# Optimization experiments

Hardware: AMD Instinct MI355X
Metric: run time of the kernel (lower is better)

## Reference

```python
import jax, jax.numpy as jnp
import numpy as np

N = 50000        # nodes
E = 800000       # edges
H = 256          # hidden_dim == output_dim
L = 5            # num_layers
NUM_ATOM_F = 9   # OGB atom categorical features
NUM_BOND_F = 3   # OGB bond categorical features
ATOM_VOCAB = 64
BOND_VOCAB = 8
G = 128          # num graphs in batch
BN_EPS = 1e-5


def setup_inputs() -> dict:
    key = jax.random.key(0)
    ks = jax.random.split(key, 24)
    s = 0.02
    inp = {
        "x_feat": jax.random.randint(ks[0], (N, NUM_ATOM_F), 0, ATOM_VOCAB),
        "edge_index": jax.random.randint(ks[1], (2, E), 0, N),
        "edge_attr_raw": jax.random.randint(ks[2], (E, NUM_BOND_F), 0, BOND_VOCAB),
        "batch": jnp.sort(jax.random.randint(ks[3], (N,), 0, G)),
        "atom_emb": s * jax.random.normal(ks[4], (NUM_ATOM_F, ATOM_VOCAB, H), jnp.float32),
        "bond_emb": s * jax.random.normal(ks[5], (NUM_BOND_F, BOND_VOCAB, H), jnp.float32),
        # per-layer GINEConv MLP: Linear(H,H) -> BN -> relu -> Linear(H,H) -> relu
        "W1": s * jax.random.normal(ks[6], (L, H, H), jnp.float32),
        "b1": jnp.zeros((L, H), jnp.float32),
        "g1": jnp.ones((L, H), jnp.float32),
        "be1": jnp.zeros((L, H), jnp.float32),
        "W2": s * jax.random.normal(ks[7], (L, H, H), jnp.float32),
        "b2": jnp.zeros((L, H), jnp.float32),
        # outer per-layer BN
        "g2": jnp.ones((L, H), jnp.float32),
        "be2": jnp.zeros((L, H), jnp.float32),
        # output head: Linear -> BN -> relu -> Linear
        "outW1": s * jax.random.normal(ks[8], (H, H), jnp.float32),
        "outb1": jnp.zeros((H,), jnp.float32),
        "outg": jnp.ones((H,), jnp.float32),
        "outbe": jnp.zeros((H,), jnp.float32),
        "outW2": s * jax.random.normal(ks[9], (H, H), jnp.float32),
        "outb2": jnp.zeros((H,), jnp.float32),
    }
    return inp


def _bn(x, g, b):
    mu = jnp.mean(x, axis=0)
    var = jnp.var(x, axis=0)
    return (x - mu) * jax.lax.rsqrt(var + BN_EPS) * g + b


def reference(x_feat, edge_index, edge_attr_raw, batch,
              atom_emb, bond_emb, W1, b1, g1, be1, W2, b2, g2, be2,
              outW1, outb1, outg, outbe, outW2, outb2):
    # Atom/Bond encoders: sum of per-feature embeddings
    x = sum(atom_emb[f][x_feat[:, f]] for f in range(NUM_ATOM_F))        # [N,H]
    e = sum(bond_emb[f][edge_attr_raw[:, f]] for f in range(NUM_BOND_F))  # [E,H]
    src, dst = edge_index[0], edge_index[1]

    for i in range(L):
        # GINEConv: (1+eps)*x + sum_j relu(x_j + e_ij), eps=0
        m = jax.nn.relu(x[src] + e)                       # [E,H]
        agg = jax.ops.segment_sum(m, dst, num_segments=N)  # [N,H]
        h = x + agg
        h = jax.nn.relu(_bn(h @ W1[i] + b1[i], g1[i], be1[i]))
        h = jax.nn.relu(h @ W2[i] + b2[i])
        x = jax.nn.relu(_bn(h, g2[i], be2[i]))

    # output head + global_add_pool
    h = jax.nn.relu(_bn(x @ outW1 + outb1, outg, outbe))
    h = h @ outW2 + outb2
    return jax.ops.segment_sum(h, batch, num_segments=G)   # [G,H]
```

## Files before the change

kernel.cpp:

```cpp
#include <hip/hip_runtime.h>
#include <hip/hip_bf16.h>

#define NN 50000
#define EE 800000
#define HH 256
#define GG 128
#define LL 5
#define NCHUNK 196
#define BN_EPS 1e-5f

typedef __attribute__((ext_vector_type(8))) short short8_t;
typedef __attribute__((ext_vector_type(4))) float f32x4;
typedef __hip_bfloat16 bf16;

#define AS1 __attribute__((address_space(1)))
#define AS3 __attribute__((address_space(3)))

__device__ __forceinline__ float bf2f(unsigned short u) {
    unsigned int i = ((unsigned int)u) << 16;
    float f;
    __builtin_memcpy(&f, &i, 4);
    return f;
}
__device__ __forceinline__ unsigned short f2bf(float f) {
    bf16 h = __float2bfloat16(f);
    unsigned short u;
    __builtin_memcpy(&u, &h, 2);
    return u;
}

__global__ __launch_bounds__(256) void k_encode(const int* __restrict__ xf,
                                                const float* __restrict__ atom_emb,
                                                bf16* __restrict__ x) {
    int n = blockIdx.x, h = threadIdx.x;
    float s = 0.f;
#pragma unroll
    for (int f = 0; f < 9; ++f) {
        int v = xf[n * 9 + f];
        s += atom_emb[((size_t)f * 64 + v) * HH + h];
    }
    x[(size_t)n * HH + h] = __float2bfloat16(s);
}

__global__ __launch_bounds__(256) void k_combo(const float* __restrict__ bond_emb,
                                               bf16* __restrict__ table) {
    int c = blockIdx.x, h = threadIdx.x;
    float v = bond_emb[(size_t)((c >> 6) & 7) * HH + h]
            + bond_emb[(size_t)(8 + ((c >> 3) & 7)) * HH + h]
            + bond_emb[(size_t)(16 + (c & 7)) * HH + h];
    table[(size_t)c * HH + h] = __float2bfloat16(v);
}

__global__ __launch_bounds__(256) void k_prepw(const float* __restrict__ W1,
                                               const float* __restrict__ W2,
                                               const float* __restrict__ oW1,
                                               const float* __restrict__ oW2,
                                               bf16* __restrict__ out) {
    int z = blockIdx.z;
    const float* src = (z < 5) ? W1 + (size_t)z * 65536
                     : (z < 10) ? W2 + (size_t)(z - 5) * 65536
                     : (z == 10) ? oW1 : oW2;
    bf16* dst = out + (size_t)z * 65536;
    __shared__ float tile[32][33];
    int kt = blockIdx.y * 32, nt = blockIdx.x * 32;
    int tx = threadIdx.x, ty = threadIdx.y;
    for (int i = ty; i < 32; i += 8) tile[i][tx] = src[(size_t)(kt + i) * 256 + nt + tx];
    __syncthreads();
    for (int i = ty; i < 32; i += 8)
        dst[(size_t)(nt + i) * 256 + kt + tx] = __float2bfloat16(tile[tx][i]);
}

__global__ __launch_bounds__(256) void k_hist(const int* __restrict__ ei, int* __restrict__ deg) {
    int e = blockIdx.x * 256 + threadIdx.x;
    if (e < EE) atomicAdd(&deg[ei[EE + e]], 1);
}

__global__ __launch_bounds__(256) void k_scan_a(const int* __restrict__ deg, int* __restrict__ ro,
                                                int* __restrict__ bsum) {
    __shared__ int sm[256];
    int b = blockIdx.x, t = threadIdx.x;
    int idx = b * 256 + t;
    int v = (idx < NN) ? deg[idx] : 0;
    sm[t] = v;
    __syncthreads();
    for (int off = 1; off < 256; off <<= 1) {
        int add = (t >= off) ? sm[t - off] : 0;
        __syncthreads();
        sm[t] += add;
        __syncthreads();
    }
    if (idx <= NN) ro[idx] = sm[t] - v;
    if (t == 255) bsum[b] = sm[255];
}

__global__ __launch_bounds__(256) void k_scan_b(int* __restrict__ bsum) {
    __shared__ int sm[256];
    int t = threadIdx.x;
    int v = (t < NCHUNK) ? bsum[t] : 0;
    sm[t] = v;
    __syncthreads();
    for (int off = 1; off < 256; off <<= 1) {
        int add = (t >= off) ? sm[t - off] : 0;
        __syncthreads();
        sm[t] += add;
        __syncthreads();
    }
    if (t < NCHUNK) bsum[t] = sm[t] - v;
}

__global__ __launch_bounds__(256) void k_scan_c(int* __restrict__ ro, const int* __restrict__ bsum,
                                                int* __restrict__ cursor) {
    int b = blockIdx.x, t = threadIdx.x;
    int idx = b * 256 + t;
    if (idx <= NN) {
        int val = ro[idx] + bsum[b];
        ro[idx] = val;
        if (idx < NN) cursor[idx] = val;
    }
}

__global__ __launch_bounds__(256) void k_scatter(const int* __restrict__ ei,
                                                 const int* __restrict__ attr,
                                                 int* __restrict__ cursor,
                                                 int2* __restrict__ ebuf) {
    int e = blockIdx.x * 256 + threadIdx.x;
    if (e < EE) {
        int d = ei[EE + e];
        int c = (attr[e * 3] << 6) | (attr[e * 3 + 1] << 3) | attr[e * 3 + 2];
        int pos = atomicAdd(&cursor[d], 1);
        ebuf[pos] = make_int2(ei[e], c);
    }
}

__global__ __launch_bounds__(256) void k_bnrelu(bf16* __restrict__ t,
                                                const float* __restrict__ sIn,
                                                const float* __restrict__ qIn,
                                                const float* __restrict__ gIn,
                                                const float* __restrict__ beIn,
                                                float invN) {
    int grp = threadIdx.x >> 6;
    int lane = threadIdx.x & 63;
    int h4 = lane * 4;
    float4 s4 = *(const float4*)(sIn + h4);
    float4 q4 = *(const float4*)(qIn + h4);
    float4 g4 = *(const float4*)(gIn + h4);
    float4 b4 = *(const float4*)(beIn + h4);
    float4 cav, cbv;
#define COEF(C)                                                 \
    { float mu = s4.C * invN;                                   \
      float var = fmaf(-mu, mu, q4.C * invN);                   \
      float a = g4.C * rsqrtf(var + BN_EPS);                    \
      cav.C = a; cbv.C = fmaf(-mu, a, b4.C); }
    COEF(x) COEF(y) COEF(z) COEF(w)
#undef COEF
    int n = blockIdx.x * 4 + grp;
    if (n >= NN) return;
    ushort4 v = *(const ushort4*)(t + (size_t)n * HH + h4);
    ushort4 o;
    o.x = f2bf(fmaxf(fmaf(bf2f(v.x), cav.x, cbv.x), 0.f));
    o.y = f2bf(fmaxf(fmaf(bf2f(v.y), cav.y, cbv.y), 0.f));
    o.z = f2bf(fmaxf(fmaf(bf2f(v.z), cav.z, cbv.z), 0.f));
    o.w = f2bf(fmaxf(fmaf(bf2f(v.w), cav.w, cbv.w), 0.f));
    *(ushort4*)(t + (size_t)n * HH + h4) = o;
}

__global__ __launch_bounds__(256) void k_aggregate(const bf16* __restrict__ u,
                                                   const int* __restrict__ ro,
                                                   const int2* __restrict__ eb,
                                                   const bf16* __restrict__ combo,
                                                   bf16* __restrict__ aggout) {
    int wid = threadIdx.x >> 6;
    int lane = threadIdx.x & 63;
    int half = lane >> 5;
    int sl = lane & 31;
    int n = blockIdx.x * 4 + wid;
    if (n >= NN) return;
    int h8 = sl * 8;
    float p0[8] = {0.f, 0.f, 0.f, 0.f, 0.f, 0.f, 0.f, 0.f};
    float p1[8] = {0.f, 0.f, 0.f, 0.f, 0.f, 0.f, 0.f, 0.f};
    int e0 = ro[n], e1 = ro[n + 1];
    int j = e0;
#define ACCUM(P, xs, cs)                                                       \
    {                                                                          \
        unsigned int xw[4] = {xs.x, xs.y, xs.z, xs.w};                         \
        unsigned int cw[4] = {cs.x, cs.y, cs.z, cs.w};                         \
        _Pragma("unroll") for (int q = 0; q < 4; ++q) {                        \
            float xlo = __uint_as_float(xw[q] << 16);                          \
            float xhi = __uint_as_float(xw[q] & 0xffff0000u);                  \
            float clo = __uint_as_float(cw[q] << 16);                          \
            float chi = __uint_as_float(cw[q] & 0xffff0000u);                  \
            P[2 * q] += fmaxf(xlo + clo, 0.f);                                 \
            P[2 * q + 1] += fmaxf(xhi + chi, 0.f);                             \
        }                                                                      \
    }
    for (; j + 4 <= e1; j += 4) {
        int2 rA = eb[j + half];
        int2 rB = eb[j + 2 + half];
        uint4 xA = *(const uint4*)(u + (size_t)rA.x * HH + h8);
        uint4 cA = *(const uint4*)(combo + ((size_t)rA.y << 8) + h8);
        uint4 xB = *(const uint4*)(u + (size_t)rB.x * HH + h8);
        uint4 cB = *(const uint4*)(combo + ((size_t)rB.y << 8) + h8);
        ACCUM(p0, xA, cA);
        ACCUM(p1, xB, cB);
    }
    for (; j < e1; j += 2) {
        int idx = j + half;
        bool v = idx < e1;
        int2 r = eb[v ? idx : e0];
        uint4 xA = *(const uint4*)(u + (size_t)r.x * HH + h8);
        uint4 cA = *(const uint4*)(combo + ((size_t)r.y << 8) + h8);
        if (v) ACCUM(p0, xA, cA);
    }
#undef ACCUM
#pragma unroll
    for (int i = 0; i < 8; ++i) {
        p0[i] += p1[i];
        p0[i] += __shfl_xor(p0[i], 32);
    }
    if (half == 0) {
        uint4 tv = *(const uint4*)(u + (size_t)n * HH + h8);
        unsigned int tw[4] = {tv.x, tv.y, tv.z, tv.w};
        unsigned int ow[4];
#pragma unroll
        for (int q = 0; q < 4; ++q) {
            float tlo = __uint_as_float(tw[q] << 16);
            float thi = __uint_as_float(tw[q] & 0xffff0000u);
            ow[q] = (unsigned int)f2bf(p0[2 * q] + tlo)
                  | ((unsigned int)f2bf(p0[2 * q + 1] + thi) << 16);
        }
        *(uint4*)(aggout + (size_t)n * HH + h8) = make_uint4(ow[0], ow[1], ow[2], ow[3]);
    }
}

struct GLds {
    uint4 a[2][512];
    uint4 b[2][1024];
    float ca[256], cb[256];
};

__device__ __forceinline__ uint4 xchunk(uint4 u, const float* ca, const float* cb, int k0) {
    float4 ca0 = *(const float4*)(ca + k0);
    float4 ca1 = *(const float4*)(ca + k0 + 4);
    float4 cb0 = *(const float4*)(cb + k0);
    float4 cb1 = *(const float4*)(cb + k0 + 4);
    float cav[8] = {ca0.x, ca0.y, ca0.z, ca0.w, ca1.x, ca1.y, ca1.z, ca1.w};
    float cbv[8] = {cb0.x, cb0.y, cb0.z, cb0.w, cb1.x, cb1.y, cb1.z, cb1.w};
    unsigned int s[4] = {u.x, u.y, u.z, u.w};
#pragma unroll
    for (int p = 0; p < 4; ++p) {
        float lo = bf2f((unsigned short)(s[p] & 0xffffu));
        float hi = bf2f((unsigned short)(s[p] >> 16));
        lo = fmaxf(fmaf(lo, cav[2 * p], cbv[2 * p]), 0.f);
        hi = fmaxf(fmaf(hi, cav[2 * p + 1], cbv[2 * p + 1]), 0.f);
        s[p] = (unsigned int)f2bf(lo) | ((unsigned int)f2bf(hi) << 16);
    }
    return make_uint4(s[0], s[1], s[2], s[3]);
}

template <bool HAS_T, bool POOL>
__global__ __launch_bounds__(512, 4) void k_gemm(const bf16* __restrict__ A,
                                                 const bf16* __restrict__ Wt,
                                                 const float* __restrict__ bias,
                                                 bf16* __restrict__ Out,
                                                 int M, int do_relu,
                                                 const float* __restrict__ sIn,
                                                 const float* __restrict__ qIn,
                                                 const float* __restrict__ gIn,
                                                 const float* __restrict__ beIn,
                                                 float invN,
                                                 float* __restrict__ ssum,
                                                 float* __restrict__ ssq,
                                                 const int* __restrict__ pbatch,
                                                 float* __restrict__ pout) {
    __shared__ GLds L;
    const int t = threadIdx.x;
    const int lane = t & 63;
    const int w = t >> 6;
    const int wr = w >> 2, wc = w & 3;
    const int m0 = blockIdx.x * 128;
    const int lhi = lane >> 4, llo = lane & 15;

    if (HAS_T) {
        if (t < 256) {
            float mu = sIn[t] * invN;
            float var = fmaf(-mu, mu, qIn[t] * invN);
            float a = gIn[t] * rsqrtf(var + BN_EPS);
            L.ca[t] = a;
            L.cb[t] = fmaf(-mu, a, beIn[t]);
        }
        __syncthreads();
    }

    const int arow_i = t & 127, akg = t >> 7;
    const bf16* aptr = A + (size_t)(m0 + arow_i) * HH + akg * 8;
    const int bcol = wc * 64 + lane;
    const bf16* bptr = Wt + (size_t)bcol * HH + wr * 8;

    f32x4 acc[4][4] = {};
    uint4 areg, anext;

#define STAGE_B(c, kb)                                                                        \
    _Pragma("unroll") for (int q = 0; q < 2; ++q) {                                           \
        __builtin_amdgcn_global_load_lds((const AS1 void*)(bptr + (kb) + q * 16),             \
                                         (AS3 void*)&L.b[c][q * 512 + w * 64], 16, 0, 0);     \
    }
#define STAGE_A_DMA(c, kb)                                                                    \
    __builtin_amdgcn_global_load_lds((const AS1 void*)(aptr + (kb)),                          \
                                     (AS3 void*)&L.a[c][w * 64], 16, 0, 0);

    STAGE_B(0, 0);
    if (HAS_T) {
        areg = *(const uint4*)(aptr + 0);
        L.a[0][t] = xchunk(areg, L.ca, L.cb, akg * 8);
    } else {
        STAGE_A_DMA(0, 0);
    }
    __syncthreads();

    int c = 0;
    for (int step = 0; step < 8; ++step) {
        const int kn = (step + 1) * 32;
        if (step < 7) {
            STAGE_B(c ^ 1, kn);
            if (HAS_T) anext = *(const uint4*)(aptr + kn);
            else STAGE_A_DMA(c ^ 1, kn);
        }
        short8_t af[4], bfv[4];
#pragma unroll
        for (int m = 0; m < 4; ++m)
            af[m] = *(const short8_t*)&L.a[c][lhi * 128 + wr * 64 + m * 16 + llo];
#pragma unroll
        for (int n = 0; n < 4; ++n)
            bfv[n] = *(const short8_t*)&L.b[c][lhi * 256 + wc * 64 + n * 16 + llo];
#pragma unroll
        for (int m = 0; m < 4; ++m)
#pragma unroll
            for (int n = 0; n < 4; ++n)
                acc[m][n] = __builtin_amdgcn_mfma_f32_16x16x32_bf16(af[m], bfv[n], acc[m][n], 0, 0, 0);
        if (HAS_T && step < 7)
            L.a[c ^ 1][t] = xchunk(anext, L.ca, L.cb, kn + akg * 8);
        __syncthreads();
        c ^= 1;
    }
#undef STAGE_B
#undef STAGE_A_DMA

    float bias_n[4];
    int col_n[4];
#pragma unroll
    for (int n = 0; n < 4; ++n) {
        col_n[n] = wc * 64 + n * 16 + llo;
        bias_n[n] = bias[col_n[n]];
    }

    if (POOL) {
        int gcur = -1;
        float pacc[4] = {0.f, 0.f, 0.f, 0.f};
#pragma unroll
        for (int m = 0; m < 4; ++m) {
#pragma unroll
            for (int j = 0; j < 4; ++j) {
                int row = m0 + wr * 64 + m * 16 + lhi * 4 + j;
                if (row < M) {
                    int g = pbatch[row];
                    if (g != gcur) {
                        if (gcur >= 0) {
#pragma unroll
                            for (int n = 0; n < 4; ++n)
                                atomicAdd(&pout[(size_t)gcur * HH + col_n[n]], pacc[n]);
                        }
                        gcur = g;
#pragma unroll
                        for (int n = 0; n < 4; ++n) pacc[n] = 0.f;
                    }
#pragma unroll
                    for (int n = 0; n < 4; ++n)
                        pacc[n] += acc[m][n][j] + bias_n[n];
                }
            }
        }
        if (gcur >= 0) {
#pragma unroll
            for (int n = 0; n < 4; ++n)
                atomicAdd(&pout[(size_t)gcur * HH + col_n[n]], pacc[n]);
        }
        return;
    }

    float ps[4] = {0.f, 0.f, 0.f, 0.f}, pq[4] = {0.f, 0.f, 0.f, 0.f};
#pragma unroll
    for (int m = 0; m < 4; ++m) {
#pragma unroll
        for (int j = 0; j < 4; ++j) {
            int row = m0 + wr * 64 + m * 16 + lhi * 4 + j;
            bool valid = row < M;
#pragma unroll
            for (int n = 0; n < 4; ++n) {
                float v = acc[m][n][j] + bias_n[n];
                if (do_relu) v = fmaxf(v, 0.f);
                if (valid) {
                    Out[(size_t)row * HH + col_n[n]] = __float2bfloat16(v);
                    ps[n] += v;
                    pq[n] = fmaf(v, v, pq[n]);
                }
            }
        }
    }

    if (ssum) {
#pragma unroll
        for (int n = 0; n < 4; ++n) {
            float s = ps[n];
            s += __shfl_xor(s, 16);
            s += __shfl_xor(s, 32);
            float q = pq[n];
            q += __shfl_xor(q, 16);
            q += __shfl_xor(q, 32);
            if (lhi == 0) {
                atomicAdd(&ssum[col_n[n]], s);
                atomicAdd(&ssq[col_n[n]], q);
            }
        }
    }
}

static size_t align256(size_t v) { return (v + 255) & ~(size_t)255; }

extern "C" void kernel_launch(void* const* d_in, const int* in_sizes, int n_in,
                              void* d_out, int out_size, void* d_ws, size_t ws_size,
                              hipStream_t stream) {
    const int* x_feat = (const int*)d_in[0];
    const int* ei = (const int*)d_in[1];
    const int* attr = (const int*)d_in[2];
    const int* batch = (const int*)d_in[3];
    const float* atom_emb = (const float*)d_in[4];
    const float* bond_emb = (const float*)d_in[5];
    const float* W1 = (const float*)d_in[6];
    const float* b1 = (const float*)d_in[7];
    const float* g1 = (const float*)d_in[8];
    const float* be1 = (const float*)d_in[9];
    const float* W2 = (const float*)d_in[10];
    const float* b2 = (const float*)d_in[11];
    const float* g2 = (const float*)d_in[12];
    const float* be2 = (const float*)d_in[13];
    const float* outW1 = (const float*)d_in[14];
    const float* outb1 = (const float*)d_in[15];
    const float* outg = (const float*)d_in[16];
    const float* outbe = (const float*)d_in[17];
    const float* outW2 = (const float*)d_in[18];
    const float* outb2 = (const float*)d_in[19];
    float* out = (float*)d_out;

    char* ws = (char*)d_ws;
    const size_t BUF_STRIDE = align256((size_t)NN * HH * 2 + 131072);
    bf16* bufA = (bf16*)ws;
    bf16* bufB = (bf16*)(ws + BUF_STRIDE);
    bf16* bufC = (bf16*)(ws + 2 * BUF_STRIDE);
    char* p = ws + 3 * BUF_STRIDE;
    int2* ebuf = (int2*)p;            p += align256((size_t)EE * sizeof(int2));
    int* deg = (int*)p;
    float* stats = (float*)(p + (size_t)NN * sizeof(int));
    const size_t ZERO_BYTES = (size_t)NN * sizeof(int) + 11 * 512 * sizeof(float);
    p += align256(ZERO_BYTES);
    int* ro = (int*)p;                p += align256((size_t)(NN + 1) * sizeof(int));
    int* cursor = (int*)p;            p += align256((size_t)NN * sizeof(int));
    int* bsum = (int*)p;              p += align256(256 * sizeof(int));
    bf16* combo = (bf16*)p;           p += align256((size_t)512 * HH * sizeof(bf16));
    bf16* wbuf = (bf16*)p;            p += align256((size_t)12 * 65536 * sizeof(bf16));

    const float invN = 1.0f / (float)NN;
    const int EBLK = (EE + 255) / 256;
    const int GBLK = (NN + 127) / 128;
    const int AGG_GRID = (NN + 3) / 4;
    const int BNR_GRID = (NN + 3) / 4;

    hipMemsetAsync(deg, 0, ZERO_BYTES, stream);
    k_hist<<<EBLK, 256, 0, stream>>>(ei, deg);
    k_scan_a<<<NCHUNK, 256, 0, stream>>>(deg, ro, bsum);
    k_scan_b<<<1, 256, 0, stream>>>(bsum);
    k_scan_c<<<NCHUNK, 256, 0, stream>>>(ro, bsum, cursor);
    k_scatter<<<EBLK, 256, 0, stream>>>(ei, attr, cursor, ebuf);
    k_combo<<<512, 256, 0, stream>>>(bond_emb, combo);
    k_prepw<<<dim3(8, 8, 12), dim3(32, 8), 0, stream>>>(W1, W2, outW1, outW2, wbuf);
    k_encode<<<NN, 256, 0, stream>>>(x_feat, atom_emb, bufA);

    for (int l = 0; l < LL; ++l) {
        float* s1 = stats + (size_t)(2 * l) * 512;
        float* q1 = s1 + 256;
        float* s2 = stats + (size_t)(2 * l + 1) * 512;
        float* q2 = s2 + 256;
        if (l > 0) {
            float* sp = stats + (size_t)(2 * l - 1) * 512;
            k_bnrelu<<<BNR_GRID, 256, 0, stream>>>(bufA, sp, sp + 256,
                                                   g2 + (size_t)(l - 1) * HH,
                                                   be2 + (size_t)(l - 1) * HH, invN);
        }
        k_aggregate<<<AGG_GRID, 256, 0, stream>>>(bufA, ro, ebuf, combo, bufB);
        k_gemm<false, false><<<GBLK, 512, 0, stream>>>(bufB, wbuf + (size_t)l * 65536,
                                                       b1 + (size_t)l * HH, bufC, NN, 0,
                                                       nullptr, nullptr, nullptr, nullptr,
                                                       invN, s1, q1, nullptr, nullptr);
        k_gemm<true, false><<<GBLK, 512, 0, stream>>>(bufC, wbuf + (size_t)(5 + l) * 65536,
                                                      b2 + (size_t)l * HH, bufA, NN, 1,
                                                      s1, q1, g1 + (size_t)l * HH,
                                                      be1 + (size_t)l * HH, invN, s2, q2,
                                                      nullptr, nullptr);
    }

    float* sP = stats + (size_t)9 * 512;
    float* sH = stats + (size_t)10 * 512;
    float* qH = sH + 256;
    k_bnrelu<<<BNR_GRID, 256, 0, stream>>>(bufA, sP, sP + 256,
                                           g2 + (size_t)4 * HH, be2 + (size_t)4 * HH, invN);
    k_gemm<false, false><<<GBLK, 512, 0, stream>>>(bufA, wbuf + (size_t)10 * 65536, outb1,
                                                   bufB, NN, 0, nullptr, nullptr, nullptr,
                                                   nullptr, invN, sH, qH, nullptr, nullptr);
    hipMemsetAsync(d_out, 0, (size_t)GG * HH * sizeof(float), stream);
    k_gemm<true, true><<<GBLK, 512, 0, stream>>>(bufB, wbuf + (size_t)11 * 65536, outb2,
                                                 bufC, NN, 0, sH, qH, outg, outbe,
                                                 invN, nullptr, nullptr, batch, out);
}
```

Baseline: 941.2 us.

## Load GEMM A fragments directly to registers and fuse final BN-ReLU into head GEMM

Adds a GEMM variant for the untransformed input that loads A fragments straight from global memory into registers, skipping the LDS staging of A. This saves LDS traffic and bank pressure, but the per-lane global loads are less coalesced. The last standalone BN+ReLU pass is folded into the first head GEMM via its on-the-fly transform, which removes one full read and write of the node features. The output memset also moves to the start of the stream.

```diff
diff --git a/kernel.cpp b/kernel.cpp
--- a/kernel.cpp
+++ b/kernel.cpp
@@ -232,6 +232,111 @@
     }
 }
 
+__global__ __launch_bounds__(512, 4) void k_gemmF(const bf16* __restrict__ A,
+                                                  const bf16* __restrict__ Wt,
+                                                  const float* __restrict__ bias,
+                                                  bf16* __restrict__ Out,
+                                                  int M,
+                                                  float* __restrict__ ssum,
+                                                  float* __restrict__ ssq) {
+    __shared__ uint4 Lb[2][1024];
+    const int t = threadIdx.x;
+    const int lane = t & 63;
+    const int w = t >> 6;
+    const int wr = w >> 2, wc = w & 3;
+    const int m0 = blockIdx.x * 128;
+    const int lhi = lane >> 4, llo = lane & 15;
+
+    const int bcol = wc * 64 + lane;
+    const bf16* bptr = Wt + (size_t)bcol * HH + wr * 8;
+
+    size_t abase[4];
+#pragma unroll
+    for (int m = 0; m < 4; ++m)
+        abase[m] = (size_t)(m0 + wr * 64 + m * 16 + llo) * HH + lhi * 8;
+
+    f32x4 acc[4][4] = {};
+    uint4 ar[4], nar[4];
+
+#define STAGE_B(c, kb)                                                                        \
+    _Pragma("unroll") for (int q = 0; q < 2; ++q) {                                           \
+        __builtin_amdgcn_global_load_lds((const AS1 void*)(bptr + (kb) + q * 16),             \
+                                         (AS3 void*)&Lb[c][q * 512 + w * 64], 16, 0, 0);      \
+    }
+
+    STAGE_B(0, 0);
+#pragma unroll
+    for (int m = 0; m < 4; ++m) ar[m] = *(const uint4*)(A + abase[m]);
+    __syncthreads();
+
+    int c = 0;
+    for (int step = 0; step < 8; ++step) {
+        const int kn = (step + 1) * 32;
+        if (step < 7) {
+            STAGE_B(c ^ 1, kn);
+#pragma unroll
+            for (int m = 0; m < 4; ++m) nar[m] = *(const uint4*)(A + abase[m] + kn);
+        }
+        short8_t af[4], bfv[4];
+#pragma unroll
+        for (int m = 0; m < 4; ++m) __builtin_memcpy(&af[m], &ar[m], 16);
+#pragma unroll
+        for (int n = 0; n < 4; ++n)
+            bfv[n] = *(const short8_t*)&Lb[c][lhi * 256 + wc * 64 + n * 16 + llo];
+#pragma unroll
+        for (int m = 0; m < 4; ++m)
+#pragma unroll
+            for (int n = 0; n < 4; ++n)
+                acc[m][n] = __builtin_amdgcn_mfma_f32_16x16x32_bf16(af[m], bfv[n], acc[m][n], 0, 0, 0);
+        if (step < 7) {
+#pragma unroll
+            for (int m = 0; m < 4; ++m) ar[m] = nar[m];
+        }
+        __syncthreads();
+        c ^= 1;
+    }
+#undef STAGE_B
+
+    float bias_n[4];
+    int col_n[4];
+#pragma unroll
+    for (int n = 0; n < 4; ++n) {
+        col_n[n] = wc * 64 + n * 16 + llo;
+        bias_n[n] = bias[col_n[n]];
+    }
+    float ps[4] = {0.f, 0.f, 0.f, 0.f}, pq[4] = {0.f, 0.f, 0.f, 0.f};
+#pragma unroll
+    for (int m = 0; m < 4; ++m) {
+#pragma unroll
+        for (int j = 0; j < 4; ++j) {
+            int row = m0 + wr * 64 + m * 16 + lhi * 4 + j;
+            bool valid = row < M;
+#pragma unroll
+            for (int n = 0; n < 4; ++n) {
+                float v = acc[m][n][j] + bias_n[n];
+                if (valid) {
+                    Out[(size_t)row * HH + col_n[n]] = __float2bfloat16(v);
+                    ps[n] += v;
+                    pq[n] = fmaf(v, v, pq[n]);
+                }
+            }
+        }
+    }
+#pragma unroll
+    for (int n = 0; n < 4; ++n) {
+        float s = ps[n];
+        s += __shfl_xor(s, 16);
+        s += __shfl_xor(s, 32);
+        float q = pq[n];
+        q += __shfl_xor(q, 16);
+        q += __shfl_xor(q, 32);
+        if (lhi == 0) {
+            atomicAdd(&ssum[col_n[n]], s);
+            atomicAdd(&ssq[col_n[n]], q);
+        }
+    }
+}
+
 struct GLds {
     uint4 a[2][512];
     uint4 b[2][1024];
@@ -257,21 +362,21 @@
     return make_uint4(s[0], s[1], s[2], s[3]);
 }
 
-template <bool HAS_T, bool POOL>
-__global__ __launch_bounds__(512, 4) void k_gemm(const bf16* __restrict__ A,
-                                                 const bf16* __restrict__ Wt,
-                                                 const float* __restrict__ bias,
-                                                 bf16* __restrict__ Out,
-                                                 int M, int do_relu,
-                                                 const float* __restrict__ sIn,
-                                                 const float* __restrict__ qIn,
-                                                 const float* __restrict__ gIn,
-                                                 const float* __restrict__ beIn,
-                                                 float invN,
-                                                 float* __restrict__ ssum,
-                                                 float* __restrict__ ssq,
-                                                 const int* __restrict__ pbatch,
-                                                 float* __restrict__ pout) {
+template <bool POOL>
+__global__ __launch_bounds__(512, 4) void k_gemmT(const bf16* __restrict__ A,
+                                                  const bf16* __restrict__ Wt,
+                                                  const float* __restrict__ bias,
+                                                  bf16* __restrict__ Out,
+                                                  int M, int do_relu,
+                                                  const float* __restrict__ sIn,
+                                                  const float* __restrict__ qIn,
+                                                  const float* __restrict__ gIn,
+                                                  const float* __restrict__ beIn,
+                                                  float invN,
+                                                  float* __restrict__ ssum,
+                                                  float* __restrict__ ssq,
+                                                  const int* __restrict__ pbatch,
+                                                  float* __restrict__ pout) {
     __shared__ GLds L;
     const int t = threadIdx.x;
     const int lane = t & 63;
@@ -280,16 +385,14 @@
     const int m0 = blockIdx.x * 128;
     const int lhi = lane >> 4, llo = lane & 15;
 
-    if (HAS_T) {
-        if (t < 256) {
-            float mu = sIn[t] * invN;
-            float var = fmaf(-mu, mu, qIn[t] * invN);
-            float a = gIn[t] * rsqrtf(var + BN_EPS);
-            L.ca[t] = a;
-            L.cb[t] = fmaf(-mu, a, beIn[t]);
-        }
-        __syncthreads();
-    }
+    if (t < 256) {
+        float mu = sIn[t] * invN;
+        float var = fmaf(-mu, mu, qIn[t] * invN);
+        float a = gIn[t] * rsqrtf(var + BN_EPS);
+        L.ca[t] = a;
+        L.cb[t] = fmaf(-mu, a, beIn[t]);
+    }
+    __syncthreads();
 
     const int arow_i = t & 127, akg = t >> 7;
     const bf16* aptr = A + (size_t)(m0 + arow_i) * HH + akg * 8;
@@ -304,17 +407,10 @@
         __builtin_amdgcn_global_load_lds((const AS1 void*)(bptr + (kb) + q * 16),             \
                                          (AS3 void*)&L.b[c][q * 512 + w * 64], 16, 0, 0);     \
     }
-#define STAGE_A_DMA(c, kb)                                                                    \
-    __builtin_amdgcn_global_load_lds((const AS1 void*)(aptr + (kb)),                          \
-                                     (AS3 void*)&L.a[c][w * 64], 16, 0, 0);
 
     STAGE_B(0, 0);
-    if (HAS_T) {
-        areg = *(const uint4*)(aptr + 0);
-        L.a[0][t] = xchunk(areg, L.ca, L.cb, akg * 8);
-    } else {
-        STAGE_A_DMA(0, 0);
-    }
+    areg = *(const uint4*)(aptr + 0);
+    L.a[0][t] = xchunk(areg, L.ca, L.cb, akg * 8);
     __syncthreads();
 
     int c = 0;
@@ -322,8 +418,7 @@
         const int kn = (step + 1) * 32;
         if (step < 7) {
             STAGE_B(c ^ 1, kn);
-            if (HAS_T) anext = *(const uint4*)(aptr + kn);
-            else STAGE_A_DMA(c ^ 1, kn);
+            anext = *(const uint4*)(aptr + kn);
         }
         short8_t af[4], bfv[4];
 #pragma unroll
@@ -337,13 +432,12 @@
 #pragma unroll
             for (int n = 0; n < 4; ++n)
                 acc[m][n] = __builtin_amdgcn_mfma_f32_16x16x32_bf16(af[m], bfv[n], acc[m][n], 0, 0, 0);
-        if (HAS_T && step < 7)
+        if (step < 7)
             L.a[c ^ 1][t] = xchunk(anext, L.ca, L.cb, kn + akg * 8);
         __syncthreads();
         c ^= 1;
     }
 #undef STAGE_B
-#undef STAGE_A_DMA
 
     float bias_n[4];
     int col_n[4];
@@ -475,6 +569,7 @@
     const int BNR_GRID = (NN + 3) / 4;
 
     hipMemsetAsync(deg, 0, ZERO_BYTES, stream);
+    hipMemsetAsync(d_out, 0, (size_t)GG * HH * sizeof(float), stream);
     k_hist<<<EBLK, 256, 0, stream>>>(ei, deg);
     k_scan_a<<<NCHUNK, 256, 0, stream>>>(deg, ro, bsum);
     k_scan_b<<<1, 256, 0, stream>>>(bsum);
@@ -496,27 +591,23 @@
                                                    be2 + (size_t)(l - 1) * HH, invN);
         }
         k_aggregate<<<AGG_GRID, 256, 0, stream>>>(bufA, ro, ebuf, combo, bufB);
-        k_gemm<false, false><<<GBLK, 512, 0, stream>>>(bufB, wbuf + (size_t)l * 65536,
-                                                       b1 + (size_t)l * HH, bufC, NN, 0,
-                                                       nullptr, nullptr, nullptr, nullptr,
-                                                       invN, s1, q1, nullptr, nullptr);
-        k_gemm<true, false><<<GBLK, 512, 0, stream>>>(bufC, wbuf + (size_t)(5 + l) * 65536,
-                                                      b2 + (size_t)l * HH, bufA, NN, 1,
-                                                      s1, q1, g1 + (size_t)l * HH,
-                                                      be1 + (size_t)l * HH, invN, s2, q2,
-                                                      nullptr, nullptr);
+        k_gemmF<<<GBLK, 512, 0, stream>>>(bufB, wbuf + (size_t)l * 65536,
+                                          b1 + (size_t)l * HH, bufC, NN, s1, q1);
+        k_gemmT<false><<<GBLK, 512, 0, stream>>>(bufC, wbuf + (size_t)(5 + l) * 65536,
+                                                 b2 + (size_t)l * HH, bufA, NN, 1,
+                                                 s1, q1, g1 + (size_t)l * HH,
+                                                 be1 + (size_t)l * HH, invN, s2, q2,
+                                                 nullptr, nullptr);
     }
 
     float* sP = stats + (size_t)9 * 512;
     float* sH = stats + (size_t)10 * 512;
     float* qH = sH + 256;
-    k_bnrelu<<<BNR_GRID, 256, 0, stream>>>(bufA, sP, sP + 256,
-                                           g2 + (size_t)4 * HH, be2 + (size_t)4 * HH, invN);
-    k_gemm<false, false><<<GBLK, 512, 0, stream>>>(bufA, wbuf + (size_t)10 * 65536, outb1,
-                                                   bufB, NN, 0, nullptr, nullptr, nullptr,
-                                                   nullptr, invN, sH, qH, nullptr, nullptr);
-    hipMemsetAsync(d_out, 0, (size_t)GG * HH * sizeof(float), stream);
-    k_gemm<true, true><<<GBLK, 512, 0, stream>>>(bufB, wbuf + (size_t)11 * 65536, outb2,
-                                                 bufC, NN, 0, sH, qH, outg, outbe,
-                                                 invN, nullptr, nullptr, batch, out);
-}
+    k_gemmT<false><<<GBLK, 512, 0, stream>>>(bufA, wbuf + (size_t)10 * 65536, outb1,
+                                             bufB, NN, 0, sP, sP + 256,
+                                             g2 + (size_t)4 * HH, be2 + (size_t)4 * HH,
+                                             invN, sH, qH, nullptr, nullptr);
+    k_gemmT<true><<<GBLK, 512, 0, stream>>>(bufB, wbuf + (size_t)11 * 65536, outb2,
+                                            bufC, NN, 0, sH, qH, outg, outbe,
+                                            invN, nullptr, nullptr, batch, out);
+}
```

Result: slower. 965.0 us (+2.5%).
